# Performance work log

Hardware: AMD Instinct MI355X
Metric: run time of the kernel (lower is better)

## Reference

```python
import jax, jax.numpy as jnp
import numpy as np

N = 100000   # nodes
E = 1600000  # edges
G = 64       # graphs in batch
IN = 5
H = 2        # GAT heads
HID = 64
NCLS = 4


def setup_inputs() -> dict:
    key = jax.random.key(0)
    ks = jax.random.split(key, 16)
    rn = lambda k, s: (jax.random.normal(k, s, dtype=jnp.float32) * 0.1)
    f32 = jnp.float32
    return {
        "x": jax.random.normal(ks[0], (N, IN), dtype=f32),
        "edge_index": jax.random.randint(ks[1], (2, E), 0, N),
        "batch": jnp.sort(jax.random.randint(ks[2], (N,), 0, G)),
        # GATConv(5 -> 64, heads=2, concat=True)
        "gat_w": rn(ks[3], (IN, H * HID)),
        "att_src": rn(ks[4], (H, HID)),
        "att_dst": rn(ks[5], (H, HID)),
        "gat_b": jnp.zeros((H * HID,), f32),
        "bn1_g": jnp.ones((H * HID,), f32), "bn1_b": jnp.zeros((H * HID,), f32),
        # SAGEConv(128 -> 64): lin_l (aggregated, with bias) + lin_r (root, no bias)
        "sage_wl": rn(ks[6], (H * HID, HID)), "sage_bl": jnp.zeros((HID,), f32),
        "sage_wr": rn(ks[7], (H * HID, HID)),
        "bn2_g": jnp.ones((HID,), f32), "bn2_b": jnp.zeros((HID,), f32),
        # GCNConv(64 -> 64)
        "gcn_w": rn(ks[8], (HID, HID)), "gcn_b": jnp.zeros((HID,), f32),
        "bn3_g": jnp.ones((HID,), f32), "bn3_b": jnp.zeros((HID,), f32),
        # classifier MLP 128 -> 64 -> 4
        "w1": rn(ks[9], (2 * HID, HID)), "b1": jnp.zeros((HID,), f32),
        "w2": rn(ks[10], (HID, NCLS)), "b2": jnp.zeros((NCLS,), f32),
    }


def _bn(h, g, b):
    # BatchNorm in training-stats mode (dropout is treated as eval/identity)
    m = h.mean(0)
    v = h.var(0)
    return (h - m) * jax.lax.rsqrt(v + 1e-5) * g + b


def _forward(x, edge_index, batch, gat_w, att_src, att_dst, gat_b, bn1_g, bn1_b,
             sage_wl, sage_bl, sage_wr, bn2_g, bn2_b, gcn_w, gcn_b, bn3_g, bn3_b,
             w1, b1, w2, b2):
    src, dst = edge_index[0], edge_index[1]  # message flows src -> dst

    # ---- GATConv (heads=2, concat) ----
    xw = (x @ gat_w).reshape(-1, H, HID)                  # [N,H,C]
    a_src = (xw * att_src).sum(-1)                        # [N,H]
    a_dst = (xw * att_dst).sum(-1)                        # [N,H]
    e = jax.nn.leaky_relu(a_src[src] + a_dst[dst], 0.2)   # [E,H]
    e_max = jax.ops.segment_max(e, dst, num_segments=N)
    e_max = jnp.where(jnp.isfinite(e_max), e_max, 0.0)
    ex = jnp.exp(e - e_max[dst])
    denom = jax.ops.segment_sum(ex, dst, num_segments=N)
    alpha = ex / (denom[dst] + 1e-16)                     # segment softmax over incoming edges
    h = jax.ops.segment_sum(xw[src] * alpha[:, :, None], dst, num_segments=N)
    h = h.reshape(-1, H * HID) + gat_b
    h = jax.nn.elu(_bn(h, bn1_g, bn1_b))

    # ---- SAGEConv (mean aggregation) ----
    deg = jax.ops.segment_sum(jnp.ones((E,), h.dtype), dst, num_segments=N)
    agg = jax.ops.segment_sum(h[src], dst, num_segments=N) / jnp.maximum(deg, 1.0)[:, None]
    h = agg @ sage_wl + sage_bl + h @ sage_wr
    h = jax.nn.elu(_bn(h, bn2_g, bn2_b))

    # ---- GCNConv (symmetric norm, self loops) ----
    hw = h @ gcn_w
    deg_sl = deg + 1.0  # degree with self loop
    dinv = jax.lax.rsqrt(deg_sl)
    msg = hw[src] * (dinv[src] * dinv[dst])[:, None]
    h = jax.ops.segment_sum(msg, dst, num_segments=N) + hw * (dinv * dinv)[:, None] + gcn_b
    h = jax.nn.elu(_bn(h, bn3_g, bn3_b))

    # ---- global mean + max pool over graphs ----
    cnt = jax.ops.segment_sum(jnp.ones((h.shape[0],), h.dtype), batch, num_segments=G)
    pmean = jax.ops.segment_sum(h, batch, num_segments=G) / jnp.maximum(cnt, 1.0)[:, None]
    pmax = jax.ops.segment_max(h, batch, num_segments=G)
    pmax = jnp.where(jnp.isfinite(pmax), pmax, 0.0)
    z = jnp.concatenate([pmean, pmax], axis=1)            # [G, 2*HID]

    # ---- classifier ----
    z = jax.nn.relu(z @ w1 + b1)
    return z @ w2 + b2                                    # [G, NCLS]


def reference(x, edge_index, batch, gat_w, att_src, att_dst, gat_b, bn1_g, bn1_b,
              sage_wl, sage_bl, sage_wr, bn2_g, bn2_b, gcn_w, gcn_b, bn3_g, bn3_b,
              w1, b1, w2, b2):
    return _forward(x, edge_index, batch, gat_w, att_src, att_dst, gat_b, bn1_g, bn1_b,
                    sage_wl, sage_bl, sage_wr, bn2_g, bn2_b, gcn_w, gcn_b, bn3_g, bn3_b,
                    w1, b1, w2, b2)
```

## Files before the change

### kernel.cpp

```cpp
#include <hip/hip_runtime.h>
#include <hip/hip_bf16.h>
#include <math.h>

#define NN 100000
#define NE 1600000
#define NG 64
#define F_IN 5
#define F1 128
#define F2 64
#define NCLS 4
#define NCHUNK 250
#define CH_E 6400
#define NBUCK ((NN + 255) / 256)
#define CAPB 6144

typedef unsigned short ushort;
typedef __bf16 bf16x8 __attribute__((ext_vector_type(8)));
typedef float f32x4 __attribute__((ext_vector_type(4)));

__device__ __forceinline__ ushort f2bf(float f) {
    unsigned u = __float_as_uint(f);
    u = (u + 0x7fffu + ((u >> 16) & 1u)) >> 16;
    return (ushort)u;
}
__device__ __forceinline__ float bf2f(ushort h) {
    return __uint_as_float(((unsigned)h) << 16);
}
__device__ __forceinline__ unsigned pack2bf(float a, float b) {
    return (unsigned)f2bf(a) | ((unsigned)f2bf(b) << 16);
}
__device__ __forceinline__ float lo_bf(unsigned p) { return __uint_as_float(p << 16); }
__device__ __forceinline__ float hi_bf(unsigned p) { return __uint_as_float(p & 0xffff0000u); }
__device__ __forceinline__ float eluf(float z) { return z > 0.f ? z : expm1f(z); }

__device__ __forceinline__ unsigned enc_f(float f) {
    unsigned b = __float_as_uint(f);
    return (b & 0x80000000u) ? ~b : (b | 0x80000000u);
}
__device__ __forceinline__ float dec_f(unsigned k) {
    unsigned b = (k & 0x80000000u) ? (k ^ 0x80000000u) : ~k;
    return __uint_as_float(b);
}
#define ENC_NEG_INF 0x007FFFFFu

__global__ void k_init(float* __restrict__ sums, float* __restrict__ psum_cnt,
                       unsigned* __restrict__ pmax) {
    int i = blockIdx.x * 256 + threadIdx.x;
    if (i < 768) sums[i] = 0.f;
    if (i < NG * F2 + NG) psum_cnt[i] = 0.f;
    if (i < NG * F2) pmax[i] = ENC_NEG_INF;
}

__global__ void k_packfrag(const float* __restrict__ wl, const float* __restrict__ wr,
                           const float* __restrict__ wg,
                           ushort* __restrict__ fragd, ushort* __restrict__ fragg) {
    int idx = blockIdx.x * 256 + threadIdx.x;
    if (idx < 16384) {
        int e = idx & 7;
        int lane = (idx >> 3) & 63;
        int ct = (idx >> 9) & 7;
        int ks = idx >> 12;
        int k = ks * 32 + (lane >> 4) * 8 + e;
        int n = ct * 16 + (lane & 15);
        float val = (n < 64) ? wl[k * 64 + n] : wr[k * 64 + (n - 64)];
        fragd[idx] = f2bf(val);
    } else if (idx < 16384 + 4096) {
        int j = idx - 16384;
        int e = j & 7;
        int lane = (j >> 3) & 63;
        int ct = (j >> 9) & 3;
        int ks = j >> 11;
        int k = ks * 32 + (lane >> 4) * 8 + e;
        int n = ct * 16 + (lane & 15);
        fragg[j] = f2bf(wg[k * 64 + n]);
    }
}

__global__ void k_hist(const int* __restrict__ ei, int* __restrict__ ghist) {
    __shared__ int lh[NBUCK];
    int c = blockIdx.x, t = threadIdx.x;
    for (int b = t; b < NBUCK; b += 256) lh[b] = 0;
    __syncthreads();
    int e0 = c * CH_E;
#pragma unroll
    for (int i = 0; i < CH_E / 256; i++) {
        int d = ei[NE + e0 + t + i * 256];
        atomicAdd(&lh[d >> 8], 1);
    }
    __syncthreads();
    for (int b = t; b < NBUCK; b += 256) ghist[c * NBUCK + b] = lh[b];
}

__global__ void k_bscan(int* __restrict__ ghist, int* __restrict__ btot) {
    __shared__ int sh[256];
    int b = blockIdx.x, t = threadIdx.x;
    int v = (t < NCHUNK) ? ghist[t * NBUCK + b] : 0;
    sh[t] = v;
    __syncthreads();
    for (int off = 1; off < 256; off <<= 1) {
        int u = (t >= off) ? sh[t - off] : 0;
        __syncthreads();
        sh[t] += u;
        __syncthreads();
    }
    if (t < NCHUNK) ghist[t * NBUCK + b] = sh[t] - v;
    if (t == 255) btot[b] = sh[255];
}

__global__ void k_bprefix(const int* __restrict__ btot, int* __restrict__ bbase,
                          int* __restrict__ rowptr) {
    __shared__ int sh[512];
    int t = threadIdx.x;
    int v = (t < NBUCK) ? btot[t] : 0;
    sh[t] = v;
    __syncthreads();
    for (int off = 1; off < 512; off <<= 1) {
        int u = (t >= off) ? sh[t - off] : 0;
        __syncthreads();
        sh[t] += u;
        __syncthreads();
    }
    if (t < NBUCK) bbase[t] = sh[t] - v;
    if (t == 0) { bbase[NBUCK] = NE; rowptr[NN] = NE; }
}

__global__ void k_scatter2(const int* __restrict__ ei, const int* __restrict__ ghist,
                           const int* __restrict__ bbase, unsigned* __restrict__ staged) {
    __shared__ int lcur[NBUCK];
    int c = blockIdx.x, t = threadIdx.x;
    for (int b = t; b < NBUCK; b += 256) lcur[b] = ghist[c * NBUCK + b] + bbase[b];
    __syncthreads();
    int e0 = c * CH_E;
#pragma unroll
    for (int i = 0; i < CH_E / 256; i++) {
        int e = e0 + t + i * 256;
        int s = ei[e];
        int d = ei[NE + e];
        int pos = atomicAdd(&lcur[d >> 8], 1);
        staged[pos] = (((unsigned)(d & 255)) << 17) | (unsigned)s;
    }
}

__global__ void k_bucket_sort(const unsigned* __restrict__ staged, const int* __restrict__ bbase,
                              int* __restrict__ rowptr, int* __restrict__ csr_src,
                              float* __restrict__ dinv) {
    __shared__ unsigned ein[CAPB];
    __shared__ unsigned sout[CAPB];
    __shared__ int lhist[256];
    __shared__ int lps[256];
    int b = blockIdx.x, t = threadIdx.x;
    int n0 = b * 256;
    int g0 = bbase[b];
    int m = bbase[b + 1] - g0;
    lhist[t] = 0;
    __syncthreads();
    if (m <= CAPB) {
        for (int i = t; i < m; i += 256) {
            unsigned u = staged[g0 + i];
            ein[i] = u;
            atomicAdd(&lhist[u >> 17], 1);
        }
        __syncthreads();
        if (n0 + t < NN) dinv[n0 + t] = rsqrtf((float)lhist[t] + 1.0f);
        lps[t] = lhist[t];
        __syncthreads();
        for (int off = 1; off < 256; off <<= 1) {
            int v = (t >= off) ? lps[t - off] : 0;
            __syncthreads();
            lps[t] += v;
            __syncthreads();
        }
        int excl = lps[t] - lhist[t];
        if (n0 + t < NN) rowptr[n0 + t] = g0 + excl;
        __syncthreads();
        lhist[t] = excl;
        __syncthreads();
        for (int i = t; i < m; i += 256) {
            unsigned u = ein[i];
            int pos = atomicAdd(&lhist[u >> 17], 1);
            sout[pos] = u & 0x1FFFFu;
        }
        __syncthreads();
        for (int i = t; i < m; i += 256) csr_src[g0 + i] = (int)sout[i];
    } else {
        for (int i = t; i < m; i += 256) {
            unsigned u = staged[g0 + i];
            atomicAdd(&lhist[u >> 17], 1);
        }
        __syncthreads();
        if (n0 + t < NN) dinv[n0 + t] = rsqrtf((float)lhist[t] + 1.0f);
        lps[t] = lhist[t];
        __syncthreads();
        for (int off = 1; off < 256; off <<= 1) {
            int v = (t >= off) ? lps[t - off] : 0;
            __syncthreads();
            lps[t] += v;
            __syncthreads();
        }
        int excl = lps[t] - lhist[t];
        if (n0 + t < NN) rowptr[n0 + t] = g0 + excl;
        __syncthreads();
        lhist[t] = excl;
        __syncthreads();
        for (int i = t; i < m; i += 256) {
            unsigned u = staged[g0 + i];
            int pos = atomicAdd(&lhist[u >> 17], 1);
            csr_src[g0 + pos] = (int)(u & 0x1FFFFu);
        }
    }
}

__global__ void k_xw(const float* __restrict__ x, const float* __restrict__ gw,
                     const float* __restrict__ aw_src, const float* __restrict__ aw_dst,
                     unsigned* __restrict__ xw32, float* __restrict__ a_src,
                     float* __restrict__ a_dst) {
    __shared__ float w[F_IN * F1];
    int t = threadIdx.x;
    for (int i = t; i < F_IN * F1; i += 256) w[i] = gw[i];
    int wv = t >> 6, lane = t & 63;
    int f0 = 2 * lane, f1 = 2 * lane + 1;
    float as0 = aw_src[f0], as1 = aw_src[f1];
    float ad0 = aw_dst[f0], ad1 = aw_dst[f1];
    __syncthreads();
    int nbase = blockIdx.x * 64;
    for (int it = 0; it < 16; it++) {
        int n = nbase + it * 4 + wv;
        if (n >= NN) break;
        float xs[F_IN];
#pragma unroll
        for (int j = 0; j < F_IN; j++) xs[j] = x[n * F_IN + j];
        float acc0 = 0.f, acc1 = 0.f;
#pragma unroll
        for (int j = 0; j < F_IN; j++) {
            acc0 += xs[j] * w[j * F1 + f0];
            acc1 += xs[j] * w[j * F1 + f1];
        }
        xw32[(size_t)n * 64 + lane] = pack2bf(acc0, acc1);
        float p = acc0 * as0 + acc1 * as1;
        float q = acc0 * ad0 + acc1 * ad1;
#pragma unroll
        for (int off = 1; off < 32; off <<= 1) {
            p += __shfl_xor(p, off);
            q += __shfl_xor(q, off);
        }
        if (lane == 0)  { a_src[n * 2 + 0] = p; a_dst[n * 2 + 0] = q; }
        if (lane == 32) { a_src[n * 2 + 1] = p; a_dst[n * 2 + 1] = q; }
    }
}

__global__ void k_gat_gather(const int* __restrict__ rowptr, const int* __restrict__ csr_src,
                             const float* __restrict__ a_src, const float* __restrict__ a_dst,
                             const unsigned* __restrict__ xw32, unsigned* __restrict__ h1p) {
    int n = blockIdx.x * 4 + (threadIdx.x >> 6);
    int lane = threadIdx.x & 63;
    if (n >= NN) return;
    int j0 = rowptr[n], j1 = rowptr[n + 1];
    int deg = j1 - j0;
    float ad0 = a_dst[n * 2 + 0], ad1 = a_dst[n * 2 + 1];
    float acc0 = 0.f, acc1 = 0.f;
    bool lo = (lane < 32);
    if (deg <= 64) {
        int sl = 0;
        float l0 = -INFINITY, l1 = -INFINITY;
        if (lane < deg) {
            sl = csr_src[j0 + lane];
            l0 = a_src[sl * 2 + 0] + ad0;
            l1 = a_src[sl * 2 + 1] + ad1;
            l0 = l0 > 0.f ? l0 : 0.2f * l0;
            l1 = l1 > 0.f ? l1 : 0.2f * l1;
        }
        float m0 = l0, m1 = l1;
#pragma unroll
        for (int off = 32; off > 0; off >>= 1) {
            m0 = fmaxf(m0, __shfl_xor(m0, off));
            m1 = fmaxf(m1, __shfl_xor(m1, off));
        }
        float e0 = 0.f, e1 = 0.f;
        if (lane < deg) { e0 = expf(l0 - m0); e1 = expf(l1 - m1); }
        float s0 = e0, s1 = e1;
#pragma unroll
        for (int off = 32; off > 0; off >>= 1) {
            s0 += __shfl_xor(s0, off);
            s1 += __shfl_xor(s1, off);
        }
        unsigned al = pack2bf(e0 / (s0 + 1e-16f), e1 / (s1 + 1e-16f));
        int e = 0;
        for (; e + 4 <= deg; e += 4) {
            int s0i = __shfl(sl, e + 0), s1i = __shfl(sl, e + 1),
                s2i = __shfl(sl, e + 2), s3i = __shfl(sl, e + 3);
            unsigned b0 = __shfl(al, e + 0), b1 = __shfl(al, e + 1),
                     b2 = __shfl(al, e + 2), b3 = __shfl(al, e + 3);
            unsigned p0 = xw32[(size_t)s0i * 64 + lane];
            unsigned p1 = xw32[(size_t)s1i * 64 + lane];
            unsigned p2 = xw32[(size_t)s2i * 64 + lane];
            unsigned p3 = xw32[(size_t)s3i * 64 + lane];
            float w0 = lo ? lo_bf(b0) : hi_bf(b0);
            float w1 = lo ? lo_bf(b1) : hi_bf(b1);
            float w2 = lo ? lo_bf(b2) : hi_bf(b2);
            float w3 = lo ? lo_bf(b3) : hi_bf(b3);
            acc0 = fmaf(lo_bf(p0), w0, acc0); acc1 = fmaf(hi_bf(p0), w0, acc1);
            acc0 = fmaf(lo_bf(p1), w1, acc0); acc1 = fmaf(hi_bf(p1), w1, acc1);
            acc0 = fmaf(lo_bf(p2), w2, acc0); acc1 = fmaf(hi_bf(p2), w2, acc1);
            acc0 = fmaf(lo_bf(p3), w3, acc0); acc1 = fmaf(hi_bf(p3), w3, acc1);
        }
        for (; e < deg; e++) {
            int s = __shfl(sl, e); unsigned b = __shfl(al, e);
            unsigned p = xw32[(size_t)s * 64 + lane];
            float w = lo ? lo_bf(b) : hi_bf(b);
            acc0 = fmaf(lo_bf(p), w, acc0);
            acc1 = fmaf(hi_bf(p), w, acc1);
        }
    } else {
        float m0 = -INFINITY, m1 = -INFINITY, s0 = 0.f, s1 = 0.f;
        for (int base = j0; base < j1; base += 64) {
            int myj = base + lane;
            float l0 = -INFINITY, l1 = -INFINITY;
            if (myj < j1) {
                int s = csr_src[myj];
                l0 = a_src[s * 2 + 0] + ad0;
                l1 = a_src[s * 2 + 1] + ad1;
                l0 = l0 > 0.f ? l0 : 0.2f * l0;
                l1 = l1 > 0.f ? l1 : 0.2f * l1;
            }
            float cm0 = l0, cm1 = l1;
#pragma unroll
            for (int off = 32; off > 0; off >>= 1) {
                cm0 = fmaxf(cm0, __shfl_xor(cm0, off));
                cm1 = fmaxf(cm1, __shfl_xor(cm1, off));
            }
            float nm0 = fmaxf(m0, cm0), nm1 = fmaxf(m1, cm1);
            float ce0 = (myj < j1) ? expf(l0 - nm0) : 0.f;
            float ce1 = (myj < j1) ? expf(l1 - nm1) : 0.f;
            float cs0 = ce0, cs1 = ce1;
#pragma unroll
            for (int off = 32; off > 0; off >>= 1) {
                cs0 += __shfl_xor(cs0, off);
                cs1 += __shfl_xor(cs1, off);
            }
            s0 = s0 * expf(m0 - nm0) + cs0;
            s1 = s1 * expf(m1 - nm1) + cs1;
            m0 = nm0; m1 = nm1;
        }
        float r0 = 1.0f / (s0 + 1e-16f), r1 = 1.0f / (s1 + 1e-16f);
        for (int base = j0; base < j1; base += 64) {
            int cnt = min(64, j1 - base);
            int myj = base + lane;
            int sl = 0; unsigned al = 0;
            if (myj < j1) {
                sl = csr_src[myj];
                float l0 = a_src[sl * 2 + 0] + ad0;
                float l1 = a_src[sl * 2 + 1] + ad1;
                l0 = l0 > 0.f ? l0 : 0.2f * l0;
                l1 = l1 > 0.f ? l1 : 0.2f * l1;
                al = pack2bf(expf(l0 - m0) * r0, expf(l1 - m1) * r1);
            }
            int e = 0;
            for (; e + 4 <= cnt; e += 4) {
                int s0i = __shfl(sl, e + 0), s1i = __shfl(sl, e + 1),
                    s2i = __shfl(sl, e + 2), s3i = __shfl(sl, e + 3);
                unsigned b0 = __shfl(al, e + 0), b1 = __shfl(al, e + 1),
                         b2 = __shfl(al, e + 2), b3 = __shfl(al, e + 3);
                unsigned p0 = xw32[(size_t)s0i * 64 + lane];
                unsigned p1 = xw32[(size_t)s1i * 64 + lane];
                unsigned p2 = xw32[(size_t)s2i * 64 + lane];
                unsigned p3 = xw32[(size_t)s3i * 64 + lane];
                float w0 = lo ? lo_bf(b0) : hi_bf(b0);
                float w1 = lo ? lo_bf(b1) : hi_bf(b1);
                float w2 = lo ? lo_bf(b2) : hi_bf(b2);
                float w3 = lo ? lo_bf(b3) : hi_bf(b3);
                acc0 = fmaf(lo_bf(p0), w0, acc0); acc1 = fmaf(hi_bf(p0), w0, acc1);
                acc0 = fmaf(lo_bf(p1), w1, acc0); acc1 = fmaf(hi_bf(p1), w1, acc1);
                acc0 = fmaf(lo_bf(p2), w2, acc0); acc1 = fmaf(hi_bf(p2), w2, acc1);
                acc0 = fmaf(lo_bf(p3), w3, acc0); acc1 = fmaf(hi_bf(p3), w3, acc1);
            }
            for (; e < cnt; e++) {
                int s = __shfl(sl, e); unsigned b = __shfl(al, e);
                unsigned p = xw32[(size_t)s * 64 + lane];
                float w = lo ? lo_bf(b) : hi_bf(b);
                acc0 = fmaf(lo_bf(p), w, acc0);
                acc1 = fmaf(hi_bf(p), w, acc1);
            }
        }
    }
    h1p[(size_t)n * 64 + lane] = pack2bf(acc0, acc1);
}

__global__ void k_bn_stats_bf(const ushort* __restrict__ h, int nfeat, float* __restrict__ sums) {
    __shared__ float sh[512];
    int t = threadIdx.x;
    int f = t & (nfeat - 1);
    int rg = t / nfeat;
    int R = 256 / nfeat;
    int rows = (NN + gridDim.x - 1) / gridDim.x;
    int rbase = blockIdx.x * rows;
    int r1 = min(NN, rbase + rows);
    float s = 0.f, ss = 0.f;
    for (int r = rbase + rg; r < r1; r += R) {
        float v = bf2f(h[(size_t)r * nfeat + f]);
        s += v; ss += v * v;
    }
    sh[t] = s; sh[256 + t] = ss;
    __syncthreads();
    if (rg == 0) {
        for (int g = 1; g < R; g++) {
            s += sh[g * nfeat + f];
            ss += sh[256 + g * nfeat + f];
        }
        atomicAdd(&sums[f], s);
        atomicAdd(&sums[nfeat + f], ss);
    }
}

__global__ void k_sage_dualgemm(const ushort* __restrict__ h1bf, const float* __restrict__ sums,
                                const float* __restrict__ g, const float* __restrict__ b,
                                const ushort* __restrict__ fragd,
                                ushort* __restrict__ u_bf, ushort* __restrict__ v_bf) {
    __shared__ uint4 sfrag[2048];
    __shared__ float sco[F1], ssh[F1];
    int t = threadIdx.x;
    const uint4* f4 = (const uint4*)fragd;
    for (int i = t; i < 2048; i += 256) sfrag[i] = f4[i];
    if (t < F1) {
        float m = sums[t] * (1.0f / NN);
        float var = sums[F1 + t] * (1.0f / NN) - m * m;
        float sc = rsqrtf(var + 1e-5f) * g[t];
        sco[t] = sc;
        ssh[t] = b[t] - m * sc;
    }
    __syncthreads();
    int w = t >> 6, lane = t & 63;
    int row0 = blockIdx.x * 64 + w * 16;
    int arow = row0 + (lane & 15);
    if (arow >= NN) arow = NN - 1;
    f32x4 acc[8];
#pragma unroll
    for (int c = 0; c < 8; c++) acc[c] = (f32x4){0.f, 0.f, 0.f, 0.f};
#pragma unroll
    for (int ks = 0; ks < 4; ks++) {
        int kb = ks * 32 + (lane >> 4) * 8;
        uint4 raw = *(const uint4*)&h1bf[(size_t)arow * F1 + kb];
        union { uint4 u; bf16x8 f; } ua;
        {
            float e0 = eluf(fmaf(lo_bf(raw.x), sco[kb + 0], ssh[kb + 0]));
            float e1 = eluf(fmaf(hi_bf(raw.x), sco[kb + 1], ssh[kb + 1]));
            float e2 = eluf(fmaf(lo_bf(raw.y), sco[kb + 2], ssh[kb + 2]));
            float e3 = eluf(fmaf(hi_bf(raw.y), sco[kb + 3], ssh[kb + 3]));
            float e4 = eluf(fmaf(lo_bf(raw.z), sco[kb + 4], ssh[kb + 4]));
            float e5 = eluf(fmaf(hi_bf(raw.z), sco[kb + 5], ssh[kb + 5]));
            float e6 = eluf(fmaf(lo_bf(raw.w), sco[kb + 6], ssh[kb + 6]));
            float e7 = eluf(fmaf(hi_bf(raw.w), sco[kb + 7], ssh[kb + 7]));
            ua.u.x = pack2bf(e0, e1); ua.u.y = pack2bf(e2, e3);
            ua.u.z = pack2bf(e4, e5); ua.u.w = pack2bf(e6, e7);
        }
#pragma unroll
        for (int ct = 0; ct < 8; ct++) {
            union { uint4 u; bf16x8 f; } ub;
            ub.u = sfrag[(ks * 8 + ct) * 64 + lane];
            acc[ct] = __builtin_amdgcn_mfma_f32_16x16x32_bf16(ua.f, ub.f, acc[ct], 0, 0, 0);
        }
    }
    int mrow0 = row0 + (lane >> 4) * 4;
    int n = lane & 15;
#pragma unroll
    for (int reg = 0; reg < 4; reg++) {
        int r = mrow0 + reg;
        if (r >= NN) continue;
#pragma unroll
        for (int ct = 0; ct < 4; ct++)
            u_bf[(size_t)r * F2 + ct * 16 + n] = f2bf(acc[ct][reg]);
#pragma unroll
        for (int ct = 4; ct < 8; ct++)
            v_bf[(size_t)r * F2 + (ct - 4) * 16 + n] = f2bf(acc[ct][reg]);
    }
}

__global__ void k_sage_gather2(const int* __restrict__ rowptr, const int* __restrict__ csr_src,
                               const ushort* __restrict__ u_bf, const ushort* __restrict__ v_bf,
                               const float* __restrict__ bl, ushort* __restrict__ h2bf) {
    int n = blockIdx.x * 4 + (threadIdx.x >> 6);
    int lane = threadIdx.x & 63;
    if (n >= NN) return;
    int j0 = rowptr[n], j1 = rowptr[n + 1];
    float a = 0.f;
    for (int base = j0; base < j1; base += 64) {
        int cnt = min(64, j1 - base);
        int myj = base + lane;
        int sl = (myj < j1) ? csr_src[myj] : 0;
        int e = 0;
        for (; e + 4 <= cnt; e += 4) {
            int s0 = __shfl(sl, e + 0), s1 = __shfl(sl, e + 1),
                s2 = __shfl(sl, e + 2), s3 = __shfl(sl, e + 3);
            float t0 = bf2f(u_bf[(size_t)s0 * F2 + lane]);
            float t1 = bf2f(u_bf[(size_t)s1 * F2 + lane]);
            float t2 = bf2f(u_bf[(size_t)s2 * F2 + lane]);
            float t3 = bf2f(u_bf[(size_t)s3 * F2 + lane]);
            a += (t0 + t1) + (t2 + t3);
        }
        for (; e < cnt; e++) {
            int s = __shfl(sl, e);
            a += bf2f(u_bf[(size_t)s * F2 + lane]);
        }
    }
    float inv = 1.0f / fmaxf((float)(j1 - j0), 1.0f);
    h2bf[(size_t)n * F2 + lane] = f2bf(a * inv + bf2f(v_bf[(size_t)n * F2 + lane]) + bl[lane]);
}

__global__ void k_gcn_gemm(const ushort* __restrict__ h2bf, const float* __restrict__ sums,
                           const float* __restrict__ g, const float* __restrict__ b,
                           const ushort* __restrict__ fragg,
                           const float* __restrict__ dinv, ushort* __restrict__ hwd_bf) {
    __shared__ uint4 sfrag[512];
    __shared__ float sco[F2], ssh[F2];
    int t = threadIdx.x;
    const uint4* f4 = (const uint4*)fragg;
    for (int i = t; i < 512; i += 256) sfrag[i] = f4[i];
    if (t < F2) {
        float m = sums[t] * (1.0f / NN);
        float var = sums[F2 + t] * (1.0f / NN) - m * m;
        float sc = rsqrtf(var + 1e-5f) * g[t];
        sco[t] = sc;
        ssh[t] = b[t] - m * sc;
    }
    __syncthreads();
    int w = t >> 6, lane = t & 63;
    int row0 = blockIdx.x * 64 + w * 16;
    int arow = row0 + (lane & 15);
    if (arow >= NN) arow = NN - 1;
    f32x4 acc[4];
#pragma unroll
    for (int c = 0; c < 4; c++) acc[c] = (f32x4){0.f, 0.f, 0.f, 0.f};
#pragma unroll
    for (int ks = 0; ks < 2; ks++) {
        int kb = ks * 32 + (lane >> 4) * 8;
        uint4 raw = *(const uint4*)&h2bf[(size_t)arow * F2 + kb];
        union { uint4 u; bf16x8 f; } ua;
        {
            float e0 = eluf(fmaf(lo_bf(raw.x), sco[kb + 0], ssh[kb + 0]));
            float e1 = eluf(fmaf(hi_bf(raw.x), sco[kb + 1], ssh[kb + 1]));
            float e2 = eluf(fmaf(lo_bf(raw.y), sco[kb + 2], ssh[kb + 2]));
            float e3 = eluf(fmaf(hi_bf(raw.y), sco[kb + 3], ssh[kb + 3]));
            float e4 = eluf(fmaf(lo_bf(raw.z), sco[kb + 4], ssh[kb + 4]));
            float e5 = eluf(fmaf(hi_bf(raw.z), sco[kb + 5], ssh[kb + 5]));
            float e6 = eluf(fmaf(lo_bf(raw.w), sco[kb + 6], ssh[kb + 6]));
            float e7 = eluf(fmaf(hi_bf(raw.w), sco[kb + 7], ssh[kb + 7]));
            ua.u.x = pack2bf(e0, e1); ua.u.y = pack2bf(e2, e3);
            ua.u.z = pack2bf(e4, e5); ua.u.w = pack2bf(e6, e7);
        }
#pragma unroll
        for (int ct = 0; ct < 4; ct++) {
            union { uint4 u; bf16x8 f; } ub;
            ub.u = sfrag[(ks * 4 + ct) * 64 + lane];
            acc[ct] = __builtin_amdgcn_mfma_f32_16x16x32_bf16(ua.f, ub.f, acc[ct], 0, 0, 0);
        }
    }
    int mrow0 = row0 + (lane >> 4) * 4;
    int n = lane & 15;
#pragma unroll
    for (int reg = 0; reg < 4; reg++) {
        int r = mrow0 + reg;
        if (r >= NN) continue;
        float d = dinv[r];
#pragma unroll
        for (int ct = 0; ct < 4; ct++)
            hwd_bf[(size_t)r * F2 + ct * 16 + n] = f2bf(acc[ct][reg] * d);
    }
}

__global__ void k_gcn_gather(const int* __restrict__ rowptr, const int* __restrict__ csr_src,
                             const ushort* __restrict__ hwd_bf, const float* __restrict__ dinv,
                             const float* __restrict__ gb, ushort* __restrict__ h3bf) {
    int n = blockIdx.x * 4 + (threadIdx.x >> 6);
    int lane = threadIdx.x & 63;
    if (n >= NN) return;
    int j0 = rowptr[n], j1 = rowptr[n + 1];
    float acc = 0.f;
    for (int base = j0; base < j1; base += 64) {
        int cnt = min(64, j1 - base);
        int myj = base + lane;
        int sl = (myj < j1) ? csr_src[myj] : 0;
        int e = 0;
        for (; e + 4 <= cnt; e += 4) {
            int s0 = __shfl(sl, e + 0), s1 = __shfl(sl, e + 1),
                s2 = __shfl(sl, e + 2), s3 = __shfl(sl, e + 3);
            float t0 = bf2f(hwd_bf[(size_t)s0 * F2 + lane]);
            float t1 = bf2f(hwd_bf[(size_t)s1 * F2 + lane]);
            float t2 = bf2f(hwd_bf[(size_t)s2 * F2 + lane]);
            float t3 = bf2f(hwd_bf[(size_t)s3 * F2 + lane]);
            acc += (t0 + t1) + (t2 + t3);
        }
        for (; e < cnt; e++) {
            int s = __shfl(sl, e);
            acc += bf2f(hwd_bf[(size_t)s * F2 + lane]);
        }
    }
    float di = dinv[n];
    acc += bf2f(hwd_bf[(size_t)n * F2 + lane]);
    h3bf[(size_t)n * F2 + lane] = f2bf(acc * di + gb[lane]);
}

__global__ void k_bn3_pool(const ushort* __restrict__ h3bf, const float* __restrict__ sums,
                           const float* __restrict__ g3, const float* __restrict__ b3,
                           const int* __restrict__ batch, float* __restrict__ psum,
                           unsigned* __restrict__ pmax, float* __restrict__ cnt) {
    int w = threadIdx.x >> 6;
    int lane = threadIdx.x & 63;
    int chunk = blockIdx.x * 4 + w;
    int nchunks = gridDim.x * 4;
    int rows = (NN + nchunks - 1) / nchunks;
    int r0 = chunk * rows;
    int r1 = min(NN, r0 + rows);
    if (r0 >= r1) return;
    float m = sums[lane] * (1.0f / NN);
    float var = sums[F2 + lane] * (1.0f / NN) - m * m;
    float sc = rsqrtf(var + 1e-5f) * g3[lane];
    float bb = b3[lane];
    int curg = batch[r0];
    float ls = 0.f, lm = -INFINITY;
    int run = 0;
    for (int r = r0; r < r1; r++) {
        int gg = batch[r];
        if (gg != curg) {
            atomicAdd(&psum[curg * F2 + lane], ls);
            atomicMax(&pmax[curg * F2 + lane], enc_f(lm));
            if (lane == 0) atomicAdd(&cnt[curg], (float)run);
            curg = gg; ls = 0.f; lm = -INFINITY; run = 0;
        }
        float v = (bf2f(h3bf[(size_t)r * F2 + lane]) - m) * sc + bb;
        v = v > 0.f ? v : expm1f(v);
        ls += v; lm = fmaxf(lm, v); run++;
    }
    atomicAdd(&psum[curg * F2 + lane], ls);
    atomicMax(&pmax[curg * F2 + lane], enc_f(lm));
    if (lane == 0) atomicAdd(&cnt[curg], (float)run);
}

__global__ void k_cls(const float* __restrict__ psum, const unsigned* __restrict__ pmax,
                      const float* __restrict__ cnt, const float* __restrict__ w1,
                      const float* __restrict__ b1, const float* __restrict__ w2,
                      const float* __restrict__ b2, float* __restrict__ out) {
    int g = blockIdx.x;
    int j = threadIdx.x;
    __shared__ float z[2 * F2];
    __shared__ float hid[F2];
    float c = fmaxf(cnt[g], 1.0f);
    z[j] = psum[g * F2 + j] / c;
    float mv = dec_f(pmax[g * F2 + j]);
    z[F2 + j] = isfinite(mv) ? mv : 0.f;
    __syncthreads();
    float acc = b1[j];
#pragma unroll 8
    for (int k = 0; k < 2 * F2; k++) acc += z[k] * w1[k * F2 + j];
    hid[j] = fmaxf(acc, 0.f);
    __syncthreads();
    if (j < NCLS) {
        float o = b2[j];
#pragma unroll 8
        for (int k = 0; k < F2; k++) o += hid[k] * w2[k * NCLS + j];
        out[g * NCLS + j] = o;
    }
}

extern "C" void kernel_launch(void* const* d_in, const int* in_sizes, int n_in,
                              void* d_out, int out_size, void* d_ws, size_t ws_size,
                              hipStream_t stream) {
    const float* x       = (const float*)d_in[0];
    const int*   ei      = (const int*)d_in[1];
    const int*   batch   = (const int*)d_in[2];
    const float* gat_w   = (const float*)d_in[3];
    const float* att_src = (const float*)d_in[4];
    const float* att_dst = (const float*)d_in[5];
    const float* bn1_g   = (const float*)d_in[7];
    const float* bn1_b   = (const float*)d_in[8];
    const float* sage_wl = (const float*)d_in[9];
    const float* sage_bl = (const float*)d_in[10];
    const float* sage_wr = (const float*)d_in[11];
    const float* bn2_g   = (const float*)d_in[12];
    const float* bn2_b   = (const float*)d_in[13];
    const float* gcn_w   = (const float*)d_in[14];
    const float* gcn_b   = (const float*)d_in[15];
    const float* bn3_g   = (const float*)d_in[16];
    const float* bn3_b   = (const float*)d_in[17];
    const float* w1      = (const float*)d_in[18];
    const float* b1      = (const float*)d_in[19];
    const float* w2      = (const float*)d_in[20];
    const float* b2      = (const float*)d_in[21];
    float* out = (float*)d_out;

    float* ws = (float*)d_ws;
    size_t o_A    = 0;
    size_t o_h1   = o_A   + (size_t)NN * F1;
    size_t o_h2   = o_h1  + (size_t)NN * F1;
    size_t o_csr  = o_h2  + (size_t)NN * F2;
    size_t o_rp   = o_csr + (size_t)NE;
    size_t o_bb   = o_rp  + (size_t)(NN + 4);
    size_t o_bt   = o_bb  + 400;
    size_t o_asrc = o_bt  + 400;
    size_t o_adst = o_asrc + (size_t)NN * 2;
    size_t o_dinv = o_adst + (size_t)NN * 2;
    size_t o_sums = o_dinv + (size_t)NN;
    size_t o_frd  = o_sums + 768;
    size_t o_frg  = o_frd  + 8192;
    size_t o_psum = o_frg  + 2048;
    size_t o_cnt  = o_psum + (size_t)NG * F2;
    size_t o_pmax = o_cnt  + (size_t)NG;

    float* A    = ws + o_A;
    float* h1r  = ws + o_h1;
    float* h2r  = ws + o_h2;
    int* csr_src = (int*)(ws + o_csr);
    int* rowptr  = (int*)(ws + o_rp);
    int* bbase   = (int*)(ws + o_bb);
    int* btot    = (int*)(ws + o_bt);
    float* asr  = ws + o_asrc;
    float* ads  = ws + o_adst;
    float* dinv = ws + o_dinv;
    float* sums1 = ws + o_sums;
    float* sums2 = sums1 + 256;
    float* sums3 = sums2 + 256;
    ushort* fragd = (ushort*)(ws + o_frd);
    ushort* fragg = (ushort*)(ws + o_frg);
    float* psum = ws + o_psum;
    float* cnt  = ws + o_cnt;
    unsigned* pmax = (unsigned*)(ws + o_pmax);

    unsigned* staged = (unsigned*)A;
    int*    ghist  = (int*)(A + 2 * 1024 * 1024);
    unsigned* xw32 = (unsigned*)A;
    ushort* u_bf   = (ushort*)A;
    ushort* v_bf   = (ushort*)(A + (size_t)NN * F2 / 2);
    ushort* hwd_bf = (ushort*)A;
    ushort* h3bf   = (ushort*)(A + (size_t)NN * F2 / 2);
    unsigned* h1p  = (unsigned*)h1r;
    ushort* h1bf   = (ushort*)h1r;
    ushort* h2bf   = (ushort*)h2r;

    k_init<<<(NG * F2 + NG + 255) / 256 + 1, 256, 0, stream>>>(sums1, psum, pmax);

    k_hist<<<NCHUNK, 256, 0, stream>>>(ei, ghist);
    k_bscan<<<NBUCK, 256, 0, stream>>>(ghist, btot);
    k_bprefix<<<1, 512, 0, stream>>>(btot, bbase, rowptr);
    k_scatter2<<<NCHUNK, 256, 0, stream>>>(ei, ghist, bbase, staged);
    k_bucket_sort<<<NBUCK, 256, 0, stream>>>(staged, bbase, rowptr, csr_src, dinv);

    k_xw<<<(NN + 63) / 64, 256, 0, stream>>>(x, gat_w, att_src, att_dst, xw32, asr, ads);
    k_gat_gather<<<(NN + 3) / 4, 256, 0, stream>>>(rowptr, csr_src, asr, ads, xw32, h1p);
    k_bn_stats_bf<<<1024, 256, 0, stream>>>(h1bf, F1, sums1);

    k_packfrag<<<(16384 + 4096 + 255) / 256, 256, 0, stream>>>(sage_wl, sage_wr, gcn_w,
                                                               fragd, fragg);
    k_sage_dualgemm<<<(NN + 63) / 64, 256, 0, stream>>>(h1bf, sums1, bn1_g, bn1_b,
                                                        fragd, u_bf, v_bf);
    k_sage_gather2<<<(NN + 3) / 4, 256, 0, stream>>>(rowptr, csr_src, u_bf, v_bf,
                                                     sage_bl, h2bf);
    k_bn_stats_bf<<<1024, 256, 0, stream>>>(h2bf, F2, sums2);

    k_gcn_gemm<<<(NN + 63) / 64, 256, 0, stream>>>(h2bf, sums2, bn2_g, bn2_b,
                                                   fragg, dinv, hwd_bf);
    k_gcn_gather<<<(NN + 3) / 4, 256, 0, stream>>>(rowptr, csr_src, hwd_bf, dinv, gcn_b, h3bf);
    k_bn_stats_bf<<<1024, 256, 0, stream>>>(h3bf, F2, sums3);

    k_bn3_pool<<<1024, 256, 0, stream>>>(h3bf, sums3, bn3_g, bn3_b, batch, psum, pmax, cnt);
    k_cls<<<NG, F2, 0, stream>>>(psum, pmax, cnt, w1, b1, w2, b2, out);
}
```

Before: 445.2 us.

## Fuse weight fragment packing into xw kernel, branchless bf16 select, unroll gathers by 8

The separate weight-packing kernel is merged into k_xw, which removes one kernel launch. The lo/hi bf16 attention-weight select in the GAT gather becomes a branchless shift-and-mask. The SAGE and GCN neighbor gathers are unrolled from 4 to 8 loads per step, giving more memory-level parallelism at the cost of more registers and a longer scalar tail loop for small degrees.

```diff
diff --git a/kernel.cpp b/kernel.cpp
--- a/kernel.cpp
+++ b/kernel.cpp
@@ -49,31 +49,6 @@
     if (i < 768) sums[i] = 0.f;
     if (i < NG * F2 + NG) psum_cnt[i] = 0.f;
     if (i < NG * F2) pmax[i] = ENC_NEG_INF;
-}
-
-__global__ void k_packfrag(const float* __restrict__ wl, const float* __restrict__ wr,
-                           const float* __restrict__ wg,
-                           ushort* __restrict__ fragd, ushort* __restrict__ fragg) {
-    int idx = blockIdx.x * 256 + threadIdx.x;
-    if (idx < 16384) {
-        int e = idx & 7;
-        int lane = (idx >> 3) & 63;
-        int ct = (idx >> 9) & 7;
-        int ks = idx >> 12;
-        int k = ks * 32 + (lane >> 4) * 8 + e;
-        int n = ct * 16 + (lane & 15);
-        float val = (n < 64) ? wl[k * 64 + n] : wr[k * 64 + (n - 64)];
-        fragd[idx] = f2bf(val);
-    } else if (idx < 16384 + 4096) {
-        int j = idx - 16384;
-        int e = j & 7;
-        int lane = (j >> 3) & 63;
-        int ct = (j >> 9) & 3;
-        int ks = j >> 11;
-        int k = ks * 32 + (lane >> 4) * 8 + e;
-        int n = ct * 16 + (lane & 15);
-        fragg[j] = f2bf(wg[k * 64 + n]);
-    }
 }
 
 __global__ void k_hist(const int* __restrict__ ei, int* __restrict__ ghist) {
@@ -212,8 +187,31 @@
 
 __global__ void k_xw(const float* __restrict__ x, const float* __restrict__ gw,
                      const float* __restrict__ aw_src, const float* __restrict__ aw_dst,
+                     const float* __restrict__ wl, const float* __restrict__ wr,
+                     const float* __restrict__ wg,
+                     ushort* __restrict__ fragd, ushort* __restrict__ fragg,
                      unsigned* __restrict__ xw32, float* __restrict__ a_src,
                      float* __restrict__ a_dst) {
+    int gid = blockIdx.x * 256 + threadIdx.x;
+    if (gid < 16384) {
+        int e = gid & 7;
+        int ln = (gid >> 3) & 63;
+        int ct = (gid >> 9) & 7;
+        int ks = gid >> 12;
+        int k = ks * 32 + (ln >> 4) * 8 + e;
+        int n = ct * 16 + (ln & 15);
+        float val = (n < 64) ? wl[k * 64 + n] : wr[k * 64 + (n - 64)];
+        fragd[gid] = f2bf(val);
+    } else if (gid < 16384 + 4096) {
+        int j = gid - 16384;
+        int e = j & 7;
+        int ln = (j >> 3) & 63;
+        int ct = (j >> 9) & 3;
+        int ks = j >> 11;
+        int k = ks * 32 + (ln >> 4) * 8 + e;
+        int n = ct * 16 + (ln & 15);
+        fragg[j] = f2bf(wg[k * 64 + n]);
+    }
     __shared__ float w[F_IN * F1];
     int t = threadIdx.x;
     for (int i = t; i < F_IN * F1; i += 256) w[i] = gw[i];
@@ -258,7 +256,7 @@
     int deg = j1 - j0;
     float ad0 = a_dst[n * 2 + 0], ad1 = a_dst[n * 2 + 1];
     float acc0 = 0.f, acc1 = 0.f;
-    bool lo = (lane < 32);
+    unsigned sh = (lane < 32) ? 16u : 0u;
     if (deg <= 64) {
         int sl = 0;
         float l0 = -INFINITY, l1 = -INFINITY;
@@ -294,10 +292,10 @@
             unsigned p1 = xw32[(size_t)s1i * 64 + lane];
             unsigned p2 = xw32[(size_t)s2i * 64 + lane];
             unsigned p3 = xw32[(size_t)s3i * 64 + lane];
-            float w0 = lo ? lo_bf(b0) : hi_bf(b0);
-            float w1 = lo ? lo_bf(b1) : hi_bf(b1);
-            float w2 = lo ? lo_bf(b2) : hi_bf(b2);
-            float w3 = lo ? lo_bf(b3) : hi_bf(b3);
+            float w0 = __uint_as_float((b0 << sh) & 0xffff0000u);
+            float w1 = __uint_as_float((b1 << sh) & 0xffff0000u);
+            float w2 = __uint_as_float((b2 << sh) & 0xffff0000u);
+            float w3 = __uint_as_float((b3 << sh) & 0xffff0000u);
             acc0 = fmaf(lo_bf(p0), w0, acc0); acc1 = fmaf(hi_bf(p0), w0, acc1);
             acc0 = fmaf(lo_bf(p1), w1, acc0); acc1 = fmaf(hi_bf(p1), w1, acc1);
             acc0 = fmaf(lo_bf(p2), w2, acc0); acc1 = fmaf(hi_bf(p2), w2, acc1);
@@ -306,7 +304,7 @@
         for (; e < deg; e++) {
             int s = __shfl(sl, e); unsigned b = __shfl(al, e);
             unsigned p = xw32[(size_t)s * 64 + lane];
-            float w = lo ? lo_bf(b) : hi_bf(b);
+            float w = __uint_as_float((b << sh) & 0xffff0000u);
             acc0 = fmaf(lo_bf(p), w, acc0);
             acc1 = fmaf(hi_bf(p), w, acc1);
         }
@@ -364,10 +362,10 @@
                 unsigned p1 = xw32[(size_t)s1i * 64 + lane];
                 unsigned p2 = xw32[(size_t)s2i * 64 + lane];
                 unsigned p3 = xw32[(size_t)s3i * 64 + lane];
-                float w0 = lo ? lo_bf(b0) : hi_bf(b0);
-                float w1 = lo ? lo_bf(b1) : hi_bf(b1);
-                float w2 = lo ? lo_bf(b2) : hi_bf(b2);
-                float w3 = lo ? lo_bf(b3) : hi_bf(b3);
+                float w0 = __uint_as_float((b0 << sh) & 0xffff0000u);
+                float w1 = __uint_as_float((b1 << sh) & 0xffff0000u);
+                float w2 = __uint_as_float((b2 << sh) & 0xffff0000u);
+                float w3 = __uint_as_float((b3 << sh) & 0xffff0000u);
                 acc0 = fmaf(lo_bf(p0), w0, acc0); acc1 = fmaf(hi_bf(p0), w0, acc1);
                 acc0 = fmaf(lo_bf(p1), w1, acc0); acc1 = fmaf(hi_bf(p1), w1, acc1);
                 acc0 = fmaf(lo_bf(p2), w2, acc0); acc1 = fmaf(hi_bf(p2), w2, acc1);
@@ -376,7 +374,7 @@
             for (; e < cnt; e++) {
                 int s = __shfl(sl, e); unsigned b = __shfl(al, e);
                 unsigned p = xw32[(size_t)s * 64 + lane];
-                float w = lo ? lo_bf(b) : hi_bf(b);
+                float w = __uint_as_float((b << sh) & 0xffff0000u);
                 acc0 = fmaf(lo_bf(p), w, acc0);
                 acc1 = fmaf(hi_bf(p), w, acc1);
             }
@@ -487,14 +485,20 @@
         int myj = base + lane;
         int sl = (myj < j1) ? csr_src[myj] : 0;
         int e = 0;
-        for (; e + 4 <= cnt; e += 4) {
+        for (; e + 8 <= cnt; e += 8) {
             int s0 = __shfl(sl, e + 0), s1 = __shfl(sl, e + 1),
-                s2 = __shfl(sl, e + 2), s3 = __shfl(sl, e + 3);
+                s2 = __shfl(sl, e + 2), s3 = __shfl(sl, e + 3),
+                s4 = __shfl(sl, e + 4), s5 = __shfl(sl, e + 5),
+                s6 = __shfl(sl, e + 6), s7 = __shfl(sl, e + 7);
             float t0 = bf2f(u_bf[(size_t)s0 * F2 + lane]);
             float t1 = bf2f(u_bf[(size_t)s1 * F2 + lane]);
             float t2 = bf2f(u_bf[(size_t)s2 * F2 + lane]);
             float t3 = bf2f(u_bf[(size_t)s3 * F2 + lane]);
-            a += (t0 + t1) + (t2 + t3);
+            float t4 = bf2f(u_bf[(size_t)s4 * F2 + lane]);
+            float t5 = bf2f(u_bf[(size_t)s5 * F2 + lane]);
+            float t6 = bf2f(u_bf[(size_t)s6 * F2 + lane]);
+            float t7 = bf2f(u_bf[(size_t)s7 * F2 + lane]);
+            a += ((t0 + t1) + (t2 + t3)) + ((t4 + t5) + (t6 + t7));
         }
         for (; e < cnt; e++) {
             int s = __shfl(sl, e);
@@ -579,14 +583,20 @@
         int myj = base + lane;
         int sl = (myj < j1) ? csr_src[myj] : 0;
         int e = 0;
-        for (; e + 4 <= cnt; e += 4) {
+        for (; e + 8 <= cnt; e += 8) {
             int s0 = __shfl(sl, e + 0), s1 = __shfl(sl, e + 1),
-                s2 = __shfl(sl, e + 2), s3 = __shfl(sl, e + 3);
+                s2 = __shfl(sl, e + 2), s3 = __shfl(sl, e + 3),
+                s4 = __shfl(sl, e + 4), s5 = __shfl(sl, e + 5),
+                s6 = __shfl(sl, e + 6), s7 = __shfl(sl, e + 7);
             float t0 = bf2f(hwd_bf[(size_t)s0 * F2 + lane]);
             float t1 = bf2f(hwd_bf[(size_t)s1 * F2 + lane]);
             float t2 = bf2f(hwd_bf[(size_t)s2 * F2 + lane]);
             float t3 = bf2f(hwd_bf[(size_t)s3 * F2 + lane]);
-            acc += (t0 + t1) + (t2 + t3);
+            float t4 = bf2f(hwd_bf[(size_t)s4 * F2 + lane]);
+            float t5 = bf2f(hwd_bf[(size_t)s5 * F2 + lane]);
+            float t6 = bf2f(hwd_bf[(size_t)s6 * F2 + lane]);
+            float t7 = bf2f(hwd_bf[(size_t)s7 * F2 + lane]);
+            acc += ((t0 + t1) + (t2 + t3)) + ((t4 + t5) + (t6 + t7));
         }
         for (; e < cnt; e++) {
             int s = __shfl(sl, e);
@@ -742,12 +752,12 @@
     k_scatter2<<<NCHUNK, 256, 0, stream>>>(ei, ghist, bbase, staged);
     k_bucket_sort<<<NBUCK, 256, 0, stream>>>(staged, bbase, rowptr, csr_src, dinv);
 
-    k_xw<<<(NN + 63) / 64, 256, 0, stream>>>(x, gat_w, att_src, att_dst, xw32, asr, ads);
+    k_xw<<<(NN + 63) / 64, 256, 0, stream>>>(x, gat_w, att_src, att_dst,
+                                             sage_wl, sage_wr, gcn_w, fragd, fragg,
+                                             xw32, asr, ads);
     k_gat_gather<<<(NN + 3) / 4, 256, 0, stream>>>(rowptr, csr_src, asr, ads, xw32, h1p);
     k_bn_stats_bf<<<1024, 256, 0, stream>>>(h1bf, F1, sums1);
 
-    k_packfrag<<<(16384 + 4096 + 255) / 256, 256, 0, stream>>>(sage_wl, sage_wr, gcn_w,
-                                                               fragd, fragg);
     k_sage_dualgemm<<<(NN + 63) / 64, 256, 0, stream>>>(h1bf, sums1, bn1_g, bn1_b,
                                                         fragd, u_bf, v_bf);
     k_sage_gather2<<<(NN + 3) / 4, 256, 0, stream>>>(rowptr, csr_src, u_bf, v_bf,
```

After: 444.8 us. About the same (-0.1%).
